# Performance work log

Measured on AMD Instinct MI355X. Metric: run time of the kernel, lower is better.

Reference implementation:

```python
import jax, jax.numpy as jnp
from jax import lax
import numpy as np

NUM_CENTROIDS = 1024
RADIUS = 0.5
K = 32
EPS = 1e-5


def _fps(xyz, num_samples):
    """Farthest point sampling. Deterministic start at index 0 (torch uses randint)."""
    B, N, _ = xyz.shape

    def step(carry, _):
        distances, farthest = carry
        centroid = jnp.take_along_axis(xyz, farthest[:, None, None], axis=1)  # [B,1,3]
        d = jnp.sum((xyz - centroid) ** 2, axis=-1)  # [B,N]
        distances = jnp.minimum(distances, d)
        nxt = jnp.argmax(distances, axis=-1).astype(jnp.int32)
        return (distances, nxt), farthest

    init = (jnp.full((B, N), jnp.inf, dtype=xyz.dtype), jnp.zeros((B,), jnp.int32))
    _, idxs = lax.scan(step, init, None, length=num_samples)  # [M,B]
    return jnp.transpose(idxs)  # [B,M]


def _ball_query(xyz, new_xyz):
    """K nearest neighbors within RADIUS; out-of-ball slots fall back to nearest."""
    d2 = (jnp.sum(new_xyz ** 2, -1)[:, :, None] + jnp.sum(xyz ** 2, -1)[:, None, :]
          - 2.0 * jnp.einsum('bmd,bnd->bmn', new_xyz, xyz))
    dist = jnp.sqrt(jnp.maximum(d2, 0.0))  # [B,M,N] cdist
    dist = jnp.where(dist > RADIUS, jnp.inf, dist)
    neg_vals, idx = lax.top_k(-dist, K)  # smallest-K distances
    mask = jnp.isinf(neg_vals)  # outside radius
    idx = jnp.where(mask, idx[:, :, 0:1], idx)
    return idx  # [B,M,K]


def _forward(xyz, features, Ws, bs, gs, bts):
    B, N, _ = xyz.shape
    cidx = lax.stop_gradient(_fps(xyz, NUM_CENTROIDS))  # [B,M] int
    new_xyz = jnp.take_along_axis(xyz, cidx[:, :, None], axis=1)  # [B,M,3]
    gidx = lax.stop_gradient(_ball_query(xyz, new_xyz))  # [B,M,K] int
    flat = gidx.reshape(B, -1)
    gxyz = jnp.take_along_axis(xyz, flat[:, :, None], axis=1).reshape(B, NUM_CENTROIDS, K, 3)
    gxyz = gxyz - new_xyz[:, :, None, :]
    gfeat = jnp.take_along_axis(features, flat[:, :, None], axis=1).reshape(B, NUM_CENTROIDS, K, -1)
    h = jnp.concatenate([gxyz, gfeat], axis=-1)  # [B,M,K,C+3]
    for W, b, g, bt in zip(Ws, bs, gs, bts):
        # 1x1 Conv1d == per-point linear over channels
        h = jnp.einsum('bmkc,oc->bmko', h, W) + b
        # BatchNorm1d in training mode: batch stats over (B*M, K), biased var
        mu = jnp.mean(h, axis=(0, 1, 2))
        var = jnp.var(h, axis=(0, 1, 2))
        h = (h - mu) * lax.rsqrt(var + EPS) * g + bt
        h = jax.nn.gelu(h, approximate=False)  # torch nn.GELU default (exact erf)
    return new_xyz, jnp.max(h, axis=2)  # [B,M,3], [B,M,128]


def setup_inputs() -> dict:
    key = jax.random.key(0)
    ks = jax.random.split(key, 8)
    B, N, C = 8, 8192, 64
    xyz = jax.random.normal(ks[0], (B, N, 3), jnp.float32)
    features = jax.random.normal(ks[1], (B, N, C), jnp.float32)
    chans = [C + 3, 64, 64, 128]
    inp = {"xyz": xyz, "features": features}
    for l in range(3):
        cin, cout = chans[l], chans[l + 1]
        inp[f"W{l + 1}"] = jax.random.normal(ks[2 + l], (cout, cin), jnp.float32) / jnp.float32(np.sqrt(cin))
        inp[f"b{l + 1}"] = jnp.zeros((cout,), jnp.float32)
        inp[f"g{l + 1}"] = jnp.ones((cout,), jnp.float32)
        inp[f"bt{l + 1}"] = jnp.zeros((cout,), jnp.float32)
    return inp


def reference(xyz, features, W1, b1, g1, bt1, W2, b2, g2, bt2, W3, b3, g3, bt3):
    return _forward(xyz, features, (W1, W2, W3), (b1, b2, b3), (g1, g2, g3), (bt1, bt2, bt3))
```

## Files before the change

### kernel.cpp

```cpp
#include <hip/hip_runtime.h>
#include <cstdint>
#include <cstddef>

#define BATCH 8
#define NPTS  8192
#define MCENT 1024
#define KNN   32
#define CFEAT 64
#define EPS_F 1e-5f

#define WS_NEED 73400320ull

__device__ __forceinline__ float erf_fast(float x) {
  float a = fabsf(x);
  float t = __builtin_amdgcn_rcpf(fmaf(0.3275911f, a, 1.0f));
  float p = fmaf(1.061405429f, t, -1.453152027f);
  p = fmaf(p, t, 1.421413741f);
  p = fmaf(p, t, -0.284496736f);
  p = fmaf(p, t, 0.254829592f);
  float e = __expf(-a * a);
  float y = fmaf(-p * t, e, 1.0f);
  return copysignf(y, x);
}
__device__ __forceinline__ float gelu_f(float x) {
  return 0.5f * x * (1.0f + erf_fast(x * 0.70710678118654752440f));
}

template<int CTRL>
__device__ __forceinline__ float dpp_max_step(float v) {
  int s = __builtin_amdgcn_update_dpp(__float_as_int(v), __float_as_int(v),
                                      CTRL, 0xf, 0xf, false);
  return fmaxf(v, __int_as_float(s));
}
__device__ __forceinline__ float wave_max_dpp(float v) {
  v = dpp_max_step<0x111>(v);
  v = dpp_max_step<0x112>(v);
  v = dpp_max_step<0x114>(v);
  v = dpp_max_step<0x118>(v);
  v = dpp_max_step<0x142>(v);
  v = dpp_max_step<0x143>(v);
  return v;
}
template<int CTRL>
__device__ __forceinline__ unsigned long long dpp_min64_step(unsigned long long v) {
  int lo = __builtin_amdgcn_update_dpp((int)(unsigned)(v & 0xffffffffull),
                                       (int)(unsigned)(v & 0xffffffffull),
                                       CTRL, 0xf, 0xf, false);
  int hi = __builtin_amdgcn_update_dpp((int)(unsigned)(v >> 32),
                                       (int)(unsigned)(v >> 32),
                                       CTRL, 0xf, 0xf, false);
  unsigned long long o = (((unsigned long long)(unsigned)hi) << 32) | (unsigned)lo;
  return o < v ? o : v;
}
__device__ __forceinline__ unsigned long long wave_min64_dpp(unsigned long long v) {
  v = dpp_min64_step<0x111>(v);
  v = dpp_min64_step<0x112>(v);
  v = dpp_min64_step<0x114>(v);
  v = dpp_min64_step<0x118>(v);
  v = dpp_min64_step<0x142>(v);
  v = dpp_min64_step<0x143>(v);
  return v;
}

template<int M, int HALF>
__device__ __forceinline__ void tree_step(float* s_, float* q_, int lane) {
  bool up = (lane & M) != 0;
#pragma unroll
  for (int j = 0; j < HALF; ++j) {
    float ks = up ? s_[j+HALF] : s_[j];
    float ds = up ? s_[j]      : s_[j+HALF];
    s_[j] = ks + __shfl_xor(ds, M, 64);
    float kq = up ? q_[j+HALF] : q_[j];
    float dq = up ? q_[j]      : q_[j+HALF];
    q_[j] = kq + __shfl_xor(dq, M, 64);
  }
}
template<int M, int HALF>
__device__ __forceinline__ void ptree_step(float* g_, int kbit) {
  bool up = (kbit & M) != 0;
#pragma unroll
  for (int j = 0; j < HALF; ++j) {
    float kv = up ? g_[j+HALF] : g_[j];
    float dv = up ? g_[j]      : g_[j+HALF];
    g_[j] = fmaxf(kv, __shfl_xor(dv, M, 64));
  }
}

#define FPS_STEPS 64
__global__ __launch_bounds__(512, 1) void fps_phase_kernel(
    const float* __restrict__ xyz, float* __restrict__ new_xyz,
    float* __restrict__ dist_ws, float* __restrict__ cst, int s0)
{
  __shared__ float pts[NPTS * 3];
  __shared__ float outb[FPS_STEPS * 3];
  __shared__ unsigned long long keys[2][8];
  int b = blockIdx.x, t = threadIdx.x;
  const float* xb = xyz + (size_t)b * NPTS * 3;

  float px[16], py[16], pz[16], dist[16];
  {
    const float4* src = (const float4*)(xb + (size_t)t * 48);
    float4 buf[12];
#pragma unroll
    for (int i = 0; i < 12; ++i) buf[i] = src[i];
    const float* f = (const float*)buf;
#pragma unroll
    for (int i = 0; i < 16; ++i) {
      px[i] = f[i*3+0]; py[i] = f[i*3+1]; pz[i] = f[i*3+2];
    }
    float4* dst = (float4*)(pts + (size_t)t * 48);
#pragma unroll
    for (int i = 0; i < 12; ++i) dst[i] = buf[i];
  }
  float* dw = dist_ws + (size_t)b * NPTS + (size_t)t * 16;
  float cx, cy, cz;
  if (s0 == 0) {
#pragma unroll
    for (int i = 0; i < 16; ++i) dist[i] = __builtin_inff();
    cx = xb[0]; cy = xb[1]; cz = xb[2];
  } else {
    float4 d0 = *(const float4*)(dw + 0);
    float4 d1 = *(const float4*)(dw + 4);
    float4 d2 = *(const float4*)(dw + 8);
    float4 d3 = *(const float4*)(dw + 12);
    dist[0]=d0.x; dist[1]=d0.y; dist[2]=d0.z; dist[3]=d0.w;
    dist[4]=d1.x; dist[5]=d1.y; dist[6]=d1.z; dist[7]=d1.w;
    dist[8]=d2.x; dist[9]=d2.y; dist[10]=d2.z; dist[11]=d2.w;
    dist[12]=d3.x; dist[13]=d3.y; dist[14]=d3.z; dist[15]=d3.w;
    cx = cst[b*3+0]; cy = cst[b*3+1]; cz = cst[b*3+2];
  }
  int lane = t & 63, wv = t >> 6;

  for (int s = 0; s < FPS_STEPS; ++s) {
    if (t == 0) { outb[s*3+0] = cx; outb[s*3+1] = cy; outb[s*3+2] = cz; }
    float bd = -1.0f; int bslot = 0;
#pragma unroll
    for (int i = 0; i < 16; ++i) {
      float dx = __fsub_rn(px[i], cx);
      float dy = __fsub_rn(py[i], cy);
      float dz = __fsub_rn(pz[i], cz);
      float d  = __fadd_rn(__fadd_rn(__fmul_rn(dx,dx), __fmul_rn(dy,dy)), __fmul_rn(dz,dz));
      float nd = fminf(dist[i], d);
      dist[i] = nd;
      if (nd > bd) { bd = nd; bslot = i; }
    }
    float w = wave_max_dpp(bd);
    float wmax = __int_as_float(__builtin_amdgcn_readlane(__float_as_int(w), 63));
    unsigned long long mk = __ballot(bd == wmax);
    int sl = __ffsll((long long)mk) - 1;
    int widx = __builtin_amdgcn_readlane(t * 16 + bslot, sl);
    if (lane == 0)
      keys[s & 1][wv] = (((unsigned long long)__float_as_uint(wmax)) << 32)
                        | (unsigned)(8191 - widx);
    __syncthreads();
    unsigned long long bk = keys[s & 1][0];
#pragma unroll
    for (int w2 = 1; w2 < 8; ++w2) {
      unsigned long long o = keys[s & 1][w2];
      if (o > bk) bk = o;
    }
    int idx = 8191 - (int)(unsigned)(bk & 0xffffffffull);
    cx = pts[idx*3+0]; cy = pts[idx*3+1]; cz = pts[idx*3+2];
  }

  *(float4*)(dw + 0)  = make_float4(dist[0], dist[1], dist[2], dist[3]);
  *(float4*)(dw + 4)  = make_float4(dist[4], dist[5], dist[6], dist[7]);
  *(float4*)(dw + 8)  = make_float4(dist[8], dist[9], dist[10], dist[11]);
  *(float4*)(dw + 12) = make_float4(dist[12], dist[13], dist[14], dist[15]);
  if (t == 0) { cst[b*3+0] = cx; cst[b*3+1] = cy; cst[b*3+2] = cz; }
  __syncthreads();
  float* ob = new_xyz + (size_t)b * MCENT * 3 + (size_t)s0 * 3;
  for (int i = t; i < FPS_STEPS * 3; i += 512) ob[i] = outb[i];
}

#define BQCAP 512
__global__ __launch_bounds__(256) void bq_kernel(const float* __restrict__ xyz,
                                                 const float* __restrict__ new_xyz,
                                                 int* __restrict__ gidx)
{
  __shared__ unsigned long long list[4][BQCAP];
  int wv = threadIdx.x >> 6, lane = threadIdx.x & 63;
  int gm = blockIdx.x * 4 + wv;
  int b  = gm >> 10;
  const float* c = new_xyz + (size_t)gm * 3;
  float c0 = c[0], c1 = c[1], c2 = c[2];
  float sc = __fadd_rn(__fadd_rn(__fmul_rn(c0,c0), __fmul_rn(c1,c1)), __fmul_rn(c2,c2));
  const float* xb = xyz + (size_t)b * NPTS * 3;

  unsigned cnt = 0;
  for (int j0 = 0; j0 < NPTS; j0 += 64) {
    int j = j0 + lane;
    float x = xb[j*3+0], y = xb[j*3+1], z = xb[j*3+2];
    float sx  = __fadd_rn(__fadd_rn(__fmul_rn(x,x), __fmul_rn(y,y)), __fmul_rn(z,z));
    float dot = __fadd_rn(__fadd_rn(__fmul_rn(c0,x), __fmul_rn(c1,y)), __fmul_rn(c2,z));
    float d2  = __fsub_rn(__fadd_rn(sc, sx), __fmul_rn(2.0f, dot));
    float dist = sqrtf(fmaxf(d2, 0.0f));
    bool in_ = (dist <= 0.5f);
    unsigned long long mask = __ballot(in_);
    unsigned off = (unsigned)__popcll(mask & ((1ull << lane) - 1ull));
    if (in_) {
      unsigned pos = cnt + off;
      if (pos < BQCAP)
        list[wv][pos] = (((unsigned long long)__float_as_uint(dist)) << 32) | (unsigned)j;
    }
    cnt += (unsigned)__popcll(mask);
  }
  if (cnt > BQCAP) cnt = BQCAP;

  unsigned long long e[8];
#pragma unroll
  for (int i = 0; i < 8; ++i) {
    unsigned pos = (unsigned)lane + ((unsigned)i << 6);
    e[i] = (pos < cnt) ? list[wv][pos] : ~0ull;
  }
#define CE_(a_, b_) { bool sw = e[b_] < e[a_]; \
                      unsigned long long lo_ = sw ? e[b_] : e[a_]; \
                      unsigned long long hi_ = sw ? e[a_] : e[b_]; \
                      e[a_] = lo_; e[b_] = hi_; }
  CE_(0,1) CE_(2,3) CE_(4,5) CE_(6,7)
  CE_(0,2) CE_(1,3) CE_(4,6) CE_(5,7)
  CE_(1,2) CE_(5,6)
  CE_(0,4) CE_(1,5) CE_(2,6) CE_(3,7)
  CE_(2,4) CE_(3,5)
  CE_(1,2) CE_(3,4) CE_(5,6)
#undef CE_

  int* gout = gidx + (size_t)gm * KNN;
  int first = 0;
  int kmax = (cnt < (unsigned)KNN) ? (int)cnt : KNN;
  for (int k = 0; k < KNN; ++k) {
    if (k < kmax) {
      unsigned long long wr = wave_min64_dpp(e[0]);
      unsigned lo32 = (unsigned)__builtin_amdgcn_readlane((int)(unsigned)(wr & 0xffffffffull), 63);
      unsigned hi32 = (unsigned)__builtin_amdgcn_readlane((int)(unsigned)(wr >> 32), 63);
      unsigned long long wmin = (((unsigned long long)hi32) << 32) | lo32;
      int idxv = (int)lo32;
      if (k == 0) first = idxv;
      if (lane == 0) gout[k] = idxv;
      bool win = (e[0] == wmin);
#pragma unroll
      for (int i = 0; i < 7; ++i) e[i] = win ? e[i+1] : e[i];
      e[7] = win ? ~0ull : e[7];
    } else {
      if (lane == 0) gout[k] = first;
    }
  }
}

__global__ __launch_bounds__(256) void l1_kernel(
    const float* __restrict__ xyz, const float* __restrict__ feats,
    const float* __restrict__ new_xyz, const int* __restrict__ gidx,
    const float* __restrict__ W, const float* __restrict__ bv,
    float* __restrict__ hout)
{
  int p  = blockIdx.x * 256 + threadIdx.x;
  int b  = p >> 15;
  int r  = p & 32767;
  int mi = r >> 5;
  int idx = gidx[p];
  const float* cc = new_xyz + (size_t)(b*MCENT + mi) * 3;
  const float* q  = xyz + (size_t)(b*NPTS + idx) * 3;
  float in[67];
  in[0] = q[0] - cc[0];
  in[1] = q[1] - cc[1];
  in[2] = q[2] - cc[2];
  const float* fr = feats + (size_t)(b*NPTS + idx) * CFEAT;
#pragma unroll
  for (int j = 0; j < 64; j += 4) {
    float4 v = *(const float4*)(fr + j);
    in[3+j] = v.x; in[4+j] = v.y; in[5+j] = v.z; in[6+j] = v.w;
  }

  float* orow = hout + (size_t)p * 64;
  for (int o4 = 0; o4 < 16; ++o4) {
    const float* w0 = W + (size_t)(o4 * 4) * 67;
    float a0 = bv[o4*4+0], a1 = bv[o4*4+1], a2 = bv[o4*4+2], a3 = bv[o4*4+3];
#pragma unroll
    for (int j = 0; j < 67; ++j) {
      float x = in[j];
      a0 = fmaf(x, w0[j],       a0);
      a1 = fmaf(x, w0[67+j],    a1);
      a2 = fmaf(x, w0[134+j],   a2);
      a3 = fmaf(x, w0[201+j],   a3);
    }
    *(float4*)(orow + o4*4) = make_float4(a0, a1, a2, a3);
  }
}

__global__ __launch_bounds__(256) void l2_kernel(
    float* __restrict__ h, const float* __restrict__ W,
    const float* __restrict__ bv, const float* __restrict__ bnp,
    const float* __restrict__ btp)
{
  int p = blockIdx.x * 256 + threadIdx.x;
  float* row = h + (size_t)p * 64;
  float in[64];
#pragma unroll
  for (int j = 0; j < 64; j += 4) {
    float4 v = *(const float4*)(row + j);
    in[j+0] = gelu_f((v.x - bnp[j+0]) * bnp[64+j+0] + btp[j+0]);
    in[j+1] = gelu_f((v.y - bnp[j+1]) * bnp[64+j+1] + btp[j+1]);
    in[j+2] = gelu_f((v.z - bnp[j+2]) * bnp[64+j+2] + btp[j+2]);
    in[j+3] = gelu_f((v.w - bnp[j+3]) * bnp[64+j+3] + btp[j+3]);
  }
  for (int o4 = 0; o4 < 16; ++o4) {
    const float* w0 = W + (size_t)(o4 * 4) * 64;
    float a0 = bv[o4*4+0], a1 = bv[o4*4+1], a2 = bv[o4*4+2], a3 = bv[o4*4+3];
#pragma unroll
    for (int j = 0; j < 64; ++j) {
      float x = in[j];
      a0 = fmaf(x, w0[j],      a0);
      a1 = fmaf(x, w0[64+j],   a1);
      a2 = fmaf(x, w0[128+j],  a2);
      a3 = fmaf(x, w0[192+j],  a3);
    }
    *(float4*)(row + o4*4) = make_float4(a0, a1, a2, a3);
  }
}

template<int C>
__global__ __launch_bounds__(256) void stats_kernel(const float* __restrict__ h,
                                                    float* __restrict__ part)
{
  constexpr int G = 256 / C;
  int t = threadIdx.x;
  int c = t % C, g = t / C;
  const float* base = h + (size_t)blockIdx.x * 512 * C;
  float s = 0.0f, ss = 0.0f;
  for (int r = g; r < 512; r += G) {
    float v = base[(size_t)r * C + c];
    s += v;
    ss = fmaf(v, v, ss);
  }
  __shared__ float ls[256], lss[256];
  ls[t] = s; lss[t] = ss;
  __syncthreads();
  if (g == 0) {
    for (int gg = 1; gg < G; ++gg) { s += ls[gg*C + c]; ss += lss[gg*C + c]; }
    part[(size_t)blockIdx.x * (2*C) + c]     = s;
    part[(size_t)blockIdx.x * (2*C) + C + c] = ss;
  }
}

template<int C>
__global__ __launch_bounds__(256) void fin_kernel(const float* __restrict__ part,
                                                  const float* __restrict__ gv,
                                                  float* __restrict__ bn)
{
  int c = blockIdx.x, t = threadIdx.x;
  float s = 0.0f, ss = 0.0f;
  for (int b2 = t; b2 < 512; b2 += 256) {
    s  += part[(size_t)b2 * (2*C) + c];
    ss += part[(size_t)b2 * (2*C) + C + c];
  }
  __shared__ float ls[256], lss[256];
  ls[t] = s; lss[t] = ss;
  __syncthreads();
  for (int k = 128; k > 0; k >>= 1) {
    if (t < k) { ls[t] += ls[t+k]; lss[t] += lss[t+k]; }
    __syncthreads();
  }
  if (t == 0) {
    const float inv_n = 1.0f / 262144.0f;
    float mu  = ls[0] * inv_n;
    float var = fmaxf(lss[0] * inv_n - mu * mu, 0.0f);
    bn[c]     = mu;
    bn[C + c] = gv[c] / sqrtf(var + EPS_F);
  }
}

__global__ __launch_bounds__(256) void act_kernel(float* __restrict__ h,
                                                  const float* __restrict__ bnp,
                                                  const float* __restrict__ btp)
{
  int p = blockIdx.x * 256 + threadIdx.x;
  float* row = h + (size_t)p * 64;
#pragma unroll
  for (int j = 0; j < 64; j += 4) {
    float4 v = *(const float4*)(row + j);
    v.x = gelu_f((v.x - bnp[j+0]) * bnp[64+j+0] + btp[j+0]);
    v.y = gelu_f((v.y - bnp[j+1]) * bnp[64+j+1] + btp[j+1]);
    v.z = gelu_f((v.z - bnp[j+2]) * bnp[64+j+2] + btp[j+2]);
    v.w = gelu_f((v.w - bnp[j+3]) * bnp[64+j+3] + btp[j+3]);
    *(float4*)(row + j) = v;
  }
}

__global__ __launch_bounds__(256, 1) void l3stats_kernel(
    const float* __restrict__ g2, const float* __restrict__ W3,
    const float* __restrict__ b3, float* __restrict__ part)
{
  int t = threadIdx.x;
  int gb = blockIdx.x >> 2, chunk = blockIdx.x & 3;
  int og0 = chunk * 32;
  int p = gb * 256 + t;
  const float* row = g2 + (size_t)p * 64;
  float in[64];
#pragma unroll
  for (int j = 0; j < 64; j += 4) {
    float4 v = *(const float4*)(row + j);
    in[j+0] = v.x; in[j+1] = v.y; in[j+2] = v.z; in[j+3] = v.w;
  }
  float s_[32], q_[32];
  for (int o4 = 0; o4 < 8; ++o4) {
    const float* w0 = W3 + (size_t)(og0 + o4 * 4) * 64;
    float a0 = b3[og0+o4*4+0], a1 = b3[og0+o4*4+1], a2 = b3[og0+o4*4+2], a3 = b3[og0+o4*4+3];
#pragma unroll
    for (int j = 0; j < 64; ++j) {
      float x = in[j];
      a0 = fmaf(x, w0[j],      a0);
      a1 = fmaf(x, w0[64+j],   a1);
      a2 = fmaf(x, w0[128+j],  a2);
      a3 = fmaf(x, w0[192+j],  a3);
    }
    int o = o4 * 4;
    s_[o]=a0; s_[o+1]=a1; s_[o+2]=a2; s_[o+3]=a3;
    q_[o]=a0*a0; q_[o+1]=a1*a1; q_[o+2]=a2*a2; q_[o+3]=a3*a3;
  }

  int wv = t >> 6, lane = t & 63;
  tree_step<1,16>(s_, q_, lane);
  tree_step<2, 8>(s_, q_, lane);
  tree_step<4, 4>(s_, q_, lane);
  tree_step<8, 2>(s_, q_, lane);
  tree_step<16,1>(s_, q_, lane);
  s_[0] += __shfl_xor(s_[0], 32, 64);
  q_[0] += __shfl_xor(q_[0], 32, 64);

  int ch = (int)(__brev((unsigned)(lane & 31)) >> 27);
  float* pw = part + ((size_t)blockIdx.x * 4 + wv) * 64;
  if (lane < 32) { pw[ch] = s_[0]; pw[32 + ch] = q_[0]; }
}

__global__ __launch_bounds__(256) void fin3_kernel(const float* __restrict__ part,
                                                   const float* __restrict__ gv,
                                                   float* __restrict__ bn)
{
  int c = blockIdx.x, t = threadIdx.x;
  int chunk = c >> 5, j = c & 31;
  float s = 0.0f, ss = 0.0f;
  for (int gb = t; gb < 1024; gb += 256) {
    int blk = gb * 4 + chunk;
#pragma unroll
    for (int wv = 0; wv < 4; ++wv) {
      const float* pw = part + ((size_t)blk * 4 + wv) * 64;
      s  += pw[j];
      ss += pw[32 + j];
    }
  }
  __shared__ float ls[256], lss[256];
  ls[t] = s; lss[t] = ss;
  __syncthreads();
  for (int k = 128; k > 0; k >>= 1) {
    if (t < k) { ls[t] += ls[t+k]; lss[t] += lss[t+k]; }
    __syncthreads();
  }
  if (t == 0) {
    const float inv_n = 1.0f / 262144.0f;
    float mu  = ls[0] * inv_n;
    float var = fmaxf(lss[0] * inv_n - mu * mu, 0.0f);
    bn[c]       = mu;
    bn[128 + c] = gv[c] / sqrtf(var + EPS_F);
  }
}

__global__ __launch_bounds__(256, 1) void pool3_kernel(
    const float* __restrict__ g2, const float* __restrict__ W3,
    const float* __restrict__ b3,
    const float* __restrict__ bnp3,
    const float* __restrict__ btp3,
    float* __restrict__ out1)
{
  int t = threadIdx.x;
  int gb = blockIdx.x >> 2, chunk = blockIdx.x & 3;
  int og0 = chunk * 32;
  int p = gb * 256 + t;
  const float* row = g2 + (size_t)p * 64;
  float in[64];
#pragma unroll
  for (int j = 0; j < 64; j += 4) {
    float4 v = *(const float4*)(row + j);
    in[j+0] = v.x; in[j+1] = v.y; in[j+2] = v.z; in[j+3] = v.w;
  }
  float g_[32];
  for (int o4 = 0; o4 < 8; ++o4) {
    const float* w0 = W3 + (size_t)(og0 + o4 * 4) * 64;
    float a0 = b3[og0+o4*4+0], a1 = b3[og0+o4*4+1], a2 = b3[og0+o4*4+2], a3 = b3[og0+o4*4+3];
#pragma unroll
    for (int j = 0; j < 64; ++j) {
      float x = in[j];
      a0 = fmaf(x, w0[j],      a0);
      a1 = fmaf(x, w0[64+j],   a1);
      a2 = fmaf(x, w0[128+j],  a2);
      a3 = fmaf(x, w0[192+j],  a3);
    }
    int oc0 = og0 + o4 * 4, o = o4 * 4;
    g_[o]   = gelu_f((a0 - bnp3[oc0+0]) * bnp3[128+oc0+0] + btp3[oc0+0]);
    g_[o+1] = gelu_f((a1 - bnp3[oc0+1]) * bnp3[128+oc0+1] + btp3[oc0+1]);
    g_[o+2] = gelu_f((a2 - bnp3[oc0+2]) * bnp3[128+oc0+2] + btp3[oc0+2]);
    g_[o+3] = gelu_f((a3 - bnp3[oc0+3]) * bnp3[128+oc0+3] + btp3[oc0+3]);
  }

  ptree_step<1,16>(g_, t);
  ptree_step<2, 8>(g_, t);
  ptree_step<4, 4>(g_, t);
  ptree_step<8, 2>(g_, t);
  ptree_step<16,1>(g_, t);

  int ch = (int)(__brev((unsigned)(t & 31)) >> 27);
  int gm = gb * 8 + (t >> 5);
  out1[(size_t)gm * 128 + og0 + ch] = g_[0];
}

__global__ void fill_kernel(float* __restrict__ out1) {
  out1[blockIdx.x * 256 + threadIdx.x] = 1.0e6f;
}

extern "C" void kernel_launch(void* const* d_in, const int* in_sizes, int n_in,
                              void* d_out, int out_size, void* d_ws, size_t ws_size,
                              hipStream_t stream)
{
  (void)in_sizes; (void)n_in; (void)out_size;
  const float* xyz   = (const float*)d_in[0];
  const float* feats = (const float*)d_in[1];
  const float* W1  = (const float*)d_in[2];
  const float* b1  = (const float*)d_in[3];
  const float* g1  = (const float*)d_in[4];
  const float* bt1 = (const float*)d_in[5];
  const float* W2  = (const float*)d_in[6];
  const float* b2  = (const float*)d_in[7];
  const float* g2  = (const float*)d_in[8];
  const float* bt2 = (const float*)d_in[9];
  const float* W3  = (const float*)d_in[10];
  const float* b3  = (const float*)d_in[11];
  const float* g3  = (const float*)d_in[12];
  const float* bt3 = (const float*)d_in[13];

  float* out0 = (float*)d_out;
  float* out1 = out0 + (size_t)BATCH * MCENT * 3;

  char* ws = (char*)d_ws;
  int*   gidx    = (int*)(ws + 0);
  float* part    = (float*)(ws + (1u << 20));
  float* bn0     = (float*)(ws + 5u * (1u << 20));
  float* bn1     = bn0 + 128;
  float* bn2     = bn0 + 256;
  float* dist_ws = (float*)(ws + 5u * (1u << 20) + 65536u);
  float* cst     = (float*)(ws + 5u * (1u << 20) + 65536u + 262144u);
  float* h1      = (float*)(ws + 6u * (1u << 20));

  if (ws_size < WS_NEED) {
    fill_kernel<<<4096, 256, 0, stream>>>(out1);
    return;
  }

  for (int ph = 0; ph < MCENT / FPS_STEPS; ++ph)
    fps_phase_kernel<<<BATCH, 512, 0, stream>>>(xyz, out0, dist_ws, cst,
                                                ph * FPS_STEPS);

  bq_kernel<<<2048, 256, 0, stream>>>(xyz, out0, gidx);
  l1_kernel<<<1024, 256, 0, stream>>>(xyz, feats, out0, gidx, W1, b1, h1);
  stats_kernel<64><<<512, 256, 0, stream>>>(h1, part);
  fin_kernel<64><<<64, 256, 0, stream>>>(part, g1, bn0);
  l2_kernel<<<1024, 256, 0, stream>>>(h1, W2, b2, bn0, bt1);
  stats_kernel<64><<<512, 256, 0, stream>>>(h1, part);
  fin_kernel<64><<<64, 256, 0, stream>>>(part, g2, bn1);
  act_kernel<<<1024, 256, 0, stream>>>(h1, bn1, bt2);
  l3stats_kernel<<<4096, 256, 0, stream>>>(h1, W3, b3, part);
  fin3_kernel<<<128, 256, 0, stream>>>(part, g3, bn2);
  pool3_kernel<<<4096, 256, 0, stream>>>(h1, W3, b3, bn2, bt3, out1);
}
```

Before: 1.623 ms.

## Pipeline ball query and layer-1 behind FPS phases in one mega kernel

Merges the FPS phase kernel, the ball query and the first linear layer into one kernel launched once per 64-centroid phase. Within a launch, blocks 0-7 advance FPS while other blocks run ball query for the previous phase's centroids and layer 1 for the phase before that. The aim is to use the CUs that sit idle while the serial 8-block FPS runs, and to drop the separate full-grid bq/l1 launches. Separately, pool3 now computes 64 output channels per block instead of 32, halving its grid and the number of input-row reloads. The costs are a larger shared-memory footprint per block, two extra launches to drain the pipeline, and ball-query/L1 work spread over far fewer blocks per phase.

```diff
diff --git a/kernel.cpp b/kernel.cpp
--- a/kernel.cpp
+++ b/kernel.cpp
@@ -87,203 +87,207 @@
 }
 
 #define FPS_STEPS 64
-__global__ __launch_bounds__(512, 1) void fps_phase_kernel(
+#define BQCAP 512
+__global__ __launch_bounds__(512, 1) void mega_kernel(
     const float* __restrict__ xyz, float* __restrict__ new_xyz,
-    float* __restrict__ dist_ws, float* __restrict__ cst, int s0)
+    float* __restrict__ dist_ws, float* __restrict__ cst, int s0,
+    int* __restrict__ gidx, const float* __restrict__ feats,
+    const float* __restrict__ W1, const float* __restrict__ b1v,
+    float* __restrict__ h1)
 {
   __shared__ float pts[NPTS * 3];
   __shared__ float outb[FPS_STEPS * 3];
   __shared__ unsigned long long keys[2][8];
-  int b = blockIdx.x, t = threadIdx.x;
-  const float* xb = xyz + (size_t)b * NPTS * 3;
-
-  float px[16], py[16], pz[16], dist[16];
-  {
-    const float4* src = (const float4*)(xb + (size_t)t * 48);
-    float4 buf[12];
-#pragma unroll
-    for (int i = 0; i < 12; ++i) buf[i] = src[i];
-    const float* f = (const float*)buf;
-#pragma unroll
-    for (int i = 0; i < 16; ++i) {
-      px[i] = f[i*3+0]; py[i] = f[i*3+1]; pz[i] = f[i*3+2];
-    }
-    float4* dst = (float4*)(pts + (size_t)t * 48);
-#pragma unroll
-    for (int i = 0; i < 12; ++i) dst[i] = buf[i];
-  }
-  float* dw = dist_ws + (size_t)b * NPTS + (size_t)t * 16;
-  float cx, cy, cz;
-  if (s0 == 0) {
-#pragma unroll
-    for (int i = 0; i < 16; ++i) dist[i] = __builtin_inff();
-    cx = xb[0]; cy = xb[1]; cz = xb[2];
-  } else {
-    float4 d0 = *(const float4*)(dw + 0);
-    float4 d1 = *(const float4*)(dw + 4);
-    float4 d2 = *(const float4*)(dw + 8);
-    float4 d3 = *(const float4*)(dw + 12);
-    dist[0]=d0.x; dist[1]=d0.y; dist[2]=d0.z; dist[3]=d0.w;
-    dist[4]=d1.x; dist[5]=d1.y; dist[6]=d1.z; dist[7]=d1.w;
-    dist[8]=d2.x; dist[9]=d2.y; dist[10]=d2.z; dist[11]=d2.w;
-    dist[12]=d3.x; dist[13]=d3.y; dist[14]=d3.z; dist[15]=d3.w;
-    cx = cst[b*3+0]; cy = cst[b*3+1]; cz = cst[b*3+2];
-  }
-  int lane = t & 63, wv = t >> 6;
-
-  for (int s = 0; s < FPS_STEPS; ++s) {
-    if (t == 0) { outb[s*3+0] = cx; outb[s*3+1] = cy; outb[s*3+2] = cz; }
-    float bd = -1.0f; int bslot = 0;
-#pragma unroll
-    for (int i = 0; i < 16; ++i) {
-      float dx = __fsub_rn(px[i], cx);
-      float dy = __fsub_rn(py[i], cy);
-      float dz = __fsub_rn(pz[i], cz);
-      float d  = __fadd_rn(__fadd_rn(__fmul_rn(dx,dx), __fmul_rn(dy,dy)), __fmul_rn(dz,dz));
-      float nd = fminf(dist[i], d);
-      dist[i] = nd;
-      if (nd > bd) { bd = nd; bslot = i; }
-    }
-    float w = wave_max_dpp(bd);
-    float wmax = __int_as_float(__builtin_amdgcn_readlane(__float_as_int(w), 63));
-    unsigned long long mk = __ballot(bd == wmax);
-    int sl = __ffsll((long long)mk) - 1;
-    int widx = __builtin_amdgcn_readlane(t * 16 + bslot, sl);
-    if (lane == 0)
-      keys[s & 1][wv] = (((unsigned long long)__float_as_uint(wmax)) << 32)
-                        | (unsigned)(8191 - widx);
+  __shared__ unsigned long long list[8][BQCAP];
+  int blk = blockIdx.x, t = threadIdx.x;
+
+  if (blk < 8) {
+    if (s0 >= MCENT) return;
+    int b = blk;
+    const float* xb = xyz + (size_t)b * NPTS * 3;
+    float px[16], py[16], pz[16], dist[16];
+    {
+      const float4* src = (const float4*)(xb + (size_t)t * 48);
+      float4 buf[12];
+#pragma unroll
+      for (int i = 0; i < 12; ++i) buf[i] = src[i];
+      const float* f = (const float*)buf;
+#pragma unroll
+      for (int i = 0; i < 16; ++i) {
+        px[i] = f[i*3+0]; py[i] = f[i*3+1]; pz[i] = f[i*3+2];
+      }
+      float4* dst = (float4*)(pts + (size_t)t * 48);
+#pragma unroll
+      for (int i = 0; i < 12; ++i) dst[i] = buf[i];
+    }
+    float* dw = dist_ws + (size_t)b * NPTS + (size_t)t * 16;
+    float cx, cy, cz;
+    if (s0 == 0) {
+#pragma unroll
+      for (int i = 0; i < 16; ++i) dist[i] = __builtin_inff();
+      cx = xb[0]; cy = xb[1]; cz = xb[2];
+    } else {
+      float4 d0 = *(const float4*)(dw + 0);
+      float4 d1 = *(const float4*)(dw + 4);
+      float4 d2 = *(const float4*)(dw + 8);
+      float4 d3 = *(const float4*)(dw + 12);
+      dist[0]=d0.x; dist[1]=d0.y; dist[2]=d0.z; dist[3]=d0.w;
+      dist[4]=d1.x; dist[5]=d1.y; dist[6]=d1.z; dist[7]=d1.w;
+      dist[8]=d2.x; dist[9]=d2.y; dist[10]=d2.z; dist[11]=d2.w;
+      dist[12]=d3.x; dist[13]=d3.y; dist[14]=d3.z; dist[15]=d3.w;
+      cx = cst[b*3+0]; cy = cst[b*3+1]; cz = cst[b*3+2];
+    }
+    int lane = t & 63, wv = t >> 6;
+
+    for (int s = 0; s < FPS_STEPS; ++s) {
+      if (t == 0) { outb[s*3+0] = cx; outb[s*3+1] = cy; outb[s*3+2] = cz; }
+      float bd = -1.0f; int bslot = 0;
+#pragma unroll
+      for (int i = 0; i < 16; ++i) {
+        float dx = __fsub_rn(px[i], cx);
+        float dy = __fsub_rn(py[i], cy);
+        float dz = __fsub_rn(pz[i], cz);
+        float d  = __fadd_rn(__fadd_rn(__fmul_rn(dx,dx), __fmul_rn(dy,dy)), __fmul_rn(dz,dz));
+        float nd = fminf(dist[i], d);
+        dist[i] = nd;
+        if (nd > bd) { bd = nd; bslot = i; }
+      }
+      float w = wave_max_dpp(bd);
+      float wmax = __int_as_float(__builtin_amdgcn_readlane(__float_as_int(w), 63));
+      unsigned long long mk = __ballot(bd == wmax);
+      int sl = __ffsll((long long)mk) - 1;
+      int widx = __builtin_amdgcn_readlane(t * 16 + bslot, sl);
+      if (lane == 0)
+        keys[s & 1][wv] = (((unsigned long long)__float_as_uint(wmax)) << 32)
+                          | (unsigned)(8191 - widx);
+      __syncthreads();
+      unsigned long long bk = keys[s & 1][0];
+#pragma unroll
+      for (int w2 = 1; w2 < 8; ++w2) {
+        unsigned long long o = keys[s & 1][w2];
+        if (o > bk) bk = o;
+      }
+      int idx = 8191 - (int)(unsigned)(bk & 0xffffffffull);
+      cx = pts[idx*3+0]; cy = pts[idx*3+1]; cz = pts[idx*3+2];
+    }
+
+    *(float4*)(dw + 0)  = make_float4(dist[0], dist[1], dist[2], dist[3]);
+    *(float4*)(dw + 4)  = make_float4(dist[4], dist[5], dist[6], dist[7]);
+    *(float4*)(dw + 8)  = make_float4(dist[8], dist[9], dist[10], dist[11]);
+    *(float4*)(dw + 12) = make_float4(dist[12], dist[13], dist[14], dist[15]);
+    if (t == 0) { cst[b*3+0] = cx; cst[b*3+1] = cy; cst[b*3+2] = cz; }
     __syncthreads();
-    unsigned long long bk = keys[s & 1][0];
-#pragma unroll
-    for (int w2 = 1; w2 < 8; ++w2) {
-      unsigned long long o = keys[s & 1][w2];
-      if (o > bk) bk = o;
-    }
-    int idx = 8191 - (int)(unsigned)(bk & 0xffffffffull);
-    cx = pts[idx*3+0]; cy = pts[idx*3+1]; cz = pts[idx*3+2];
-  }
-
-  *(float4*)(dw + 0)  = make_float4(dist[0], dist[1], dist[2], dist[3]);
-  *(float4*)(dw + 4)  = make_float4(dist[4], dist[5], dist[6], dist[7]);
-  *(float4*)(dw + 8)  = make_float4(dist[8], dist[9], dist[10], dist[11]);
-  *(float4*)(dw + 12) = make_float4(dist[12], dist[13], dist[14], dist[15]);
-  if (t == 0) { cst[b*3+0] = cx; cst[b*3+1] = cy; cst[b*3+2] = cz; }
-  __syncthreads();
-  float* ob = new_xyz + (size_t)b * MCENT * 3 + (size_t)s0 * 3;
-  for (int i = t; i < FPS_STEPS * 3; i += 512) ob[i] = outb[i];
-}
-
-#define BQCAP 512
-__global__ __launch_bounds__(256) void bq_kernel(const float* __restrict__ xyz,
-                                                 const float* __restrict__ new_xyz,
-                                                 int* __restrict__ gidx)
-{
-  __shared__ unsigned long long list[4][BQCAP];
-  int wv = threadIdx.x >> 6, lane = threadIdx.x & 63;
-  int gm = blockIdx.x * 4 + wv;
-  int b  = gm >> 10;
-  const float* c = new_xyz + (size_t)gm * 3;
-  float c0 = c[0], c1 = c[1], c2 = c[2];
-  float sc = __fadd_rn(__fadd_rn(__fmul_rn(c0,c0), __fmul_rn(c1,c1)), __fmul_rn(c2,c2));
-  const float* xb = xyz + (size_t)b * NPTS * 3;
-
-  unsigned cnt = 0;
-  for (int j0 = 0; j0 < NPTS; j0 += 64) {
-    int j = j0 + lane;
-    float x = xb[j*3+0], y = xb[j*3+1], z = xb[j*3+2];
-    float sx  = __fadd_rn(__fadd_rn(__fmul_rn(x,x), __fmul_rn(y,y)), __fmul_rn(z,z));
-    float dot = __fadd_rn(__fadd_rn(__fmul_rn(c0,x), __fmul_rn(c1,y)), __fmul_rn(c2,z));
-    float d2  = __fsub_rn(__fadd_rn(sc, sx), __fmul_rn(2.0f, dot));
-    float dist = sqrtf(fmaxf(d2, 0.0f));
-    bool in_ = (dist <= 0.5f);
-    unsigned long long mask = __ballot(in_);
-    unsigned off = (unsigned)__popcll(mask & ((1ull << lane) - 1ull));
-    if (in_) {
-      unsigned pos = cnt + off;
-      if (pos < BQCAP)
-        list[wv][pos] = (((unsigned long long)__float_as_uint(dist)) << 32) | (unsigned)j;
-    }
-    cnt += (unsigned)__popcll(mask);
-  }
-  if (cnt > BQCAP) cnt = BQCAP;
-
-  unsigned long long e[8];
-#pragma unroll
-  for (int i = 0; i < 8; ++i) {
-    unsigned pos = (unsigned)lane + ((unsigned)i << 6);
-    e[i] = (pos < cnt) ? list[wv][pos] : ~0ull;
-  }
+    float* ob = new_xyz + (size_t)b * MCENT * 3 + (size_t)s0 * 3;
+    for (int i = t; i < FPS_STEPS * 3; i += 512) ob[i] = outb[i];
+
+  } else if (blk < 72) {
+    int ph = s0 - FPS_STEPS;
+    if (ph < 0 || ph >= MCENT) return;
+    int wv = t >> 6, lane = t & 63;
+    int c  = (blk - 8) * 8 + wv;
+    int b  = c >> 6;
+    int ci = ph + (c & 63);
+    int gm = b * MCENT + ci;
+    const float* cc = new_xyz + (size_t)gm * 3;
+    float c0 = cc[0], c1 = cc[1], c2 = cc[2];
+    float sc = __fadd_rn(__fadd_rn(__fmul_rn(c0,c0), __fmul_rn(c1,c1)), __fmul_rn(c2,c2));
+    const float* xb = xyz + (size_t)b * NPTS * 3;
+
+    unsigned cnt = 0;
+    for (int j0 = 0; j0 < NPTS; j0 += 64) {
+      int j = j0 + lane;
+      float x = xb[j*3+0], y = xb[j*3+1], z = xb[j*3+2];
+      float sx  = __fadd_rn(__fadd_rn(__fmul_rn(x,x), __fmul_rn(y,y)), __fmul_rn(z,z));
+      float dot = __fadd_rn(__fadd_rn(__fmul_rn(c0,x), __fmul_rn(c1,y)), __fmul_rn(c2,z));
+      float d2  = __fsub_rn(__fadd_rn(sc, sx), __fmul_rn(2.0f, dot));
+      float dist = sqrtf(fmaxf(d2, 0.0f));
+      bool in_ = (dist <= 0.5f);
+      unsigned long long mask = __ballot(in_);
+      unsigned off = (unsigned)__popcll(mask & ((1ull << lane) - 1ull));
+      if (in_) {
+        unsigned pos = cnt + off;
+        if (pos < BQCAP)
+          list[wv][pos] = (((unsigned long long)__float_as_uint(dist)) << 32) | (unsigned)j;
+      }
+      cnt += (unsigned)__popcll(mask);
+    }
+    if (cnt > BQCAP) cnt = BQCAP;
+
+    unsigned long long e[8];
+#pragma unroll
+    for (int i = 0; i < 8; ++i) {
+      unsigned pos = (unsigned)lane + ((unsigned)i << 6);
+      e[i] = (pos < cnt) ? list[wv][pos] : ~0ull;
+    }
 #define CE_(a_, b_) { bool sw = e[b_] < e[a_]; \
                       unsigned long long lo_ = sw ? e[b_] : e[a_]; \
                       unsigned long long hi_ = sw ? e[a_] : e[b_]; \
                       e[a_] = lo_; e[b_] = hi_; }
-  CE_(0,1) CE_(2,3) CE_(4,5) CE_(6,7)
-  CE_(0,2) CE_(1,3) CE_(4,6) CE_(5,7)
-  CE_(1,2) CE_(5,6)
-  CE_(0,4) CE_(1,5) CE_(2,6) CE_(3,7)
-  CE_(2,4) CE_(3,5)
-  CE_(1,2) CE_(3,4) CE_(5,6)
+    CE_(0,1) CE_(2,3) CE_(4,5) CE_(6,7)
+    CE_(0,2) CE_(1,3) CE_(4,6) CE_(5,7)
+    CE_(1,2) CE_(5,6)
+    CE_(0,4) CE_(1,5) CE_(2,6) CE_(3,7)
+    CE_(2,4) CE_(3,5)
+    CE_(1,2) CE_(3,4) CE_(5,6)
 #undef CE_
 
-  int* gout = gidx + (size_t)gm * KNN;
-  int first = 0;
-  int kmax = (cnt < (unsigned)KNN) ? (int)cnt : KNN;
-  for (int k = 0; k < KNN; ++k) {
-    if (k < kmax) {
-      unsigned long long wr = wave_min64_dpp(e[0]);
-      unsigned lo32 = (unsigned)__builtin_amdgcn_readlane((int)(unsigned)(wr & 0xffffffffull), 63);
-      unsigned hi32 = (unsigned)__builtin_amdgcn_readlane((int)(unsigned)(wr >> 32), 63);
-      unsigned long long wmin = (((unsigned long long)hi32) << 32) | lo32;
-      int idxv = (int)lo32;
-      if (k == 0) first = idxv;
-      if (lane == 0) gout[k] = idxv;
-      bool win = (e[0] == wmin);
-#pragma unroll
-      for (int i = 0; i < 7; ++i) e[i] = win ? e[i+1] : e[i];
-      e[7] = win ? ~0ull : e[7];
-    } else {
-      if (lane == 0) gout[k] = first;
-    }
-  }
-}
-
-__global__ __launch_bounds__(256) void l1_kernel(
-    const float* __restrict__ xyz, const float* __restrict__ feats,
-    const float* __restrict__ new_xyz, const int* __restrict__ gidx,
-    const float* __restrict__ W, const float* __restrict__ bv,
-    float* __restrict__ hout)
-{
-  int p  = blockIdx.x * 256 + threadIdx.x;
-  int b  = p >> 15;
-  int r  = p & 32767;
-  int mi = r >> 5;
-  int idx = gidx[p];
-  const float* cc = new_xyz + (size_t)(b*MCENT + mi) * 3;
-  const float* q  = xyz + (size_t)(b*NPTS + idx) * 3;
-  float in[67];
-  in[0] = q[0] - cc[0];
-  in[1] = q[1] - cc[1];
-  in[2] = q[2] - cc[2];
-  const float* fr = feats + (size_t)(b*NPTS + idx) * CFEAT;
-#pragma unroll
-  for (int j = 0; j < 64; j += 4) {
-    float4 v = *(const float4*)(fr + j);
-    in[3+j] = v.x; in[4+j] = v.y; in[5+j] = v.z; in[6+j] = v.w;
-  }
-
-  float* orow = hout + (size_t)p * 64;
-  for (int o4 = 0; o4 < 16; ++o4) {
-    const float* w0 = W + (size_t)(o4 * 4) * 67;
-    float a0 = bv[o4*4+0], a1 = bv[o4*4+1], a2 = bv[o4*4+2], a3 = bv[o4*4+3];
-#pragma unroll
-    for (int j = 0; j < 67; ++j) {
-      float x = in[j];
-      a0 = fmaf(x, w0[j],       a0);
-      a1 = fmaf(x, w0[67+j],    a1);
-      a2 = fmaf(x, w0[134+j],   a2);
-      a3 = fmaf(x, w0[201+j],   a3);
-    }
-    *(float4*)(orow + o4*4) = make_float4(a0, a1, a2, a3);
+    int* gout = gidx + (size_t)gm * KNN;
+    int first = 0;
+    int kmax = (cnt < (unsigned)KNN) ? (int)cnt : KNN;
+    for (int k = 0; k < KNN; ++k) {
+      if (k < kmax) {
+        unsigned long long wr = wave_min64_dpp(e[0]);
+        unsigned lo32 = (unsigned)__builtin_amdgcn_readlane((int)(unsigned)(wr & 0xffffffffull), 63);
+        unsigned hi32 = (unsigned)__builtin_amdgcn_readlane((int)(unsigned)(wr >> 32), 63);
+        unsigned long long wmin = (((unsigned long long)hi32) << 32) | lo32;
+        int idxv = (int)lo32;
+        if (k == 0) first = idxv;
+        if (lane == 0) gout[k] = idxv;
+        bool win = (e[0] == wmin);
+#pragma unroll
+        for (int i = 0; i < 7; ++i) e[i] = win ? e[i+1] : e[i];
+        e[7] = win ? ~0ull : e[7];
+      } else {
+        if (lane == 0) gout[k] = first;
+      }
+    }
+
+  } else if (blk < 104) {
+    int ph = s0 - 2 * FPS_STEPS;
+    if (ph < 0) return;
+    int row = (blk - 72) * 512 + t;
+    int c   = row >> 5;
+    int k   = row & 31;
+    int b   = c >> 6;
+    int ci  = ph + (c & 63);
+    int p   = b * (MCENT * KNN) + ci * KNN + k;
+    int idx = gidx[p];
+    const float* cc = new_xyz + (size_t)(b * MCENT + ci) * 3;
+    const float* q  = xyz + (size_t)(b * NPTS + idx) * 3;
+    float in[67];
+    in[0] = q[0] - cc[0];
+    in[1] = q[1] - cc[1];
+    in[2] = q[2] - cc[2];
+    const float* fr = feats + (size_t)(b * NPTS + idx) * CFEAT;
+#pragma unroll
+    for (int j = 0; j < 64; j += 4) {
+      float4 v = *(const float4*)(fr + j);
+      in[3+j] = v.x; in[4+j] = v.y; in[5+j] = v.z; in[6+j] = v.w;
+    }
+    float* orow = h1 + (size_t)p * 64;
+    for (int o4 = 0; o4 < 16; ++o4) {
+      const float* w0 = W1 + (size_t)(o4 * 4) * 67;
+      float a0 = b1v[o4*4+0], a1 = b1v[o4*4+1], a2 = b1v[o4*4+2], a3 = b1v[o4*4+3];
+#pragma unroll
+      for (int j = 0; j < 67; ++j) {
+        float x = in[j];
+        a0 = fmaf(x, w0[j],       a0);
+        a1 = fmaf(x, w0[67+j],    a1);
+        a2 = fmaf(x, w0[134+j],   a2);
+        a3 = fmaf(x, w0[201+j],   a3);
+      }
+      *(float4*)(orow + o4*4) = make_float4(a0, a1, a2, a3);
+    }
   }
 }
 
@@ -472,8 +476,7 @@
     float* __restrict__ out1)
 {
   int t = threadIdx.x;
-  int gb = blockIdx.x >> 2, chunk = blockIdx.x & 3;
-  int og0 = chunk * 32;
+  int gb = blockIdx.x >> 1, og0 = (blockIdx.x & 1) * 64;
   int p = gb * 256 + t;
   const float* row = g2 + (size_t)p * 64;
   float in[64];
@@ -482,8 +485,8 @@
     float4 v = *(const float4*)(row + j);
     in[j+0] = v.x; in[j+1] = v.y; in[j+2] = v.z; in[j+3] = v.w;
   }
-  float g_[32];
-  for (int o4 = 0; o4 < 8; ++o4) {
+  float g_[64];
+  for (int o4 = 0; o4 < 16; ++o4) {
     const float* w0 = W3 + (size_t)(og0 + o4 * 4) * 64;
     float a0 = b3[og0+o4*4+0], a1 = b3[og0+o4*4+1], a2 = b3[og0+o4*4+2], a3 = b3[og0+o4*4+3];
 #pragma unroll
@@ -501,15 +504,16 @@
     g_[o+3] = gelu_f((a3 - bnp3[oc0+3]) * bnp3[128+oc0+3] + btp3[oc0+3]);
   }
 
-  ptree_step<1,16>(g_, t);
-  ptree_step<2, 8>(g_, t);
-  ptree_step<4, 4>(g_, t);
-  ptree_step<8, 2>(g_, t);
-  ptree_step<16,1>(g_, t);
-
-  int ch = (int)(__brev((unsigned)(t & 31)) >> 27);
+  ptree_step<1,32>(g_, t);
+  ptree_step<2,16>(g_, t);
+  ptree_step<4, 8>(g_, t);
+  ptree_step<8, 4>(g_, t);
+  ptree_step<16,2>(g_, t);
+
+  int ch0 = (int)(__brev((unsigned)(t & 31)) >> 27) * 2;
   int gm = gb * 8 + (t >> 5);
-  out1[(size_t)gm * 128 + og0 + ch] = g_[0];
+  out1[(size_t)gm * 128 + og0 + ch0]     = g_[0];
+  out1[(size_t)gm * 128 + og0 + ch0 + 1] = g_[1];
 }
 
 __global__ void fill_kernel(float* __restrict__ out1) {
@@ -554,12 +558,10 @@
     return;
   }
 
-  for (int ph = 0; ph < MCENT / FPS_STEPS; ++ph)
-    fps_phase_kernel<<<BATCH, 512, 0, stream>>>(xyz, out0, dist_ws, cst,
-                                                ph * FPS_STEPS);
-
-  bq_kernel<<<2048, 256, 0, stream>>>(xyz, out0, gidx);
-  l1_kernel<<<1024, 256, 0, stream>>>(xyz, feats, out0, gidx, W1, b1, h1);
+  for (int s0 = 0; s0 <= MCENT + FPS_STEPS; s0 += FPS_STEPS)
+    mega_kernel<<<104, 512, 0, stream>>>(xyz, out0, dist_ws, cst, s0,
+                                         gidx, feats, W1, b1, h1);
+
   stats_kernel<64><<<512, 256, 0, stream>>>(h1, part);
   fin_kernel<64><<<64, 256, 0, stream>>>(part, g1, bn0);
   l2_kernel<<<1024, 256, 0, stream>>>(h1, W2, b2, bn0, bt1);
@@ -568,5 +570,5 @@
   act_kernel<<<1024, 256, 0, stream>>>(h1, bn1, bt2);
   l3stats_kernel<<<4096, 256, 0, stream>>>(h1, W3, b3, part);
   fin3_kernel<<<128, 256, 0, stream>>>(part, g3, bn2);
-  pool3_kernel<<<4096, 256, 0, stream>>>(h1, W3, b3, bn2, bt3, out1);
-}
+  pool3_kernel<<<2048, 256, 0, stream>>>(h1, W3, b3, bn2, bt3, out1);
+}
```

New measurement: 1.554 ms. -4.3%, faster.
